# Kernel tuning notes

Hardware: AMD Instinct MI355X
Metric: run time of the kernel (lower is better)

The kernel has to match this reference:

```python
import jax, jax.numpy as jnp
import numpy as np

D_MODEL = 1024
N_HEADS = 16
D_K = D_MODEL // N_HEADS

def setup_inputs() -> dict:
    key = jax.random.key(0)
    ks = jax.random.split(key, 9)
    s = 1.0 / np.sqrt(D_MODEL)
    inp = {"x": jax.random.normal(ks[0], (2, 2048, D_MODEL), dtype=jnp.float32)}
    for i, name in enumerate(["q", "k", "v", "o"]):
        inp[f"W{name}"] = jax.random.uniform(ks[1 + i], (D_MODEL, D_MODEL), dtype=jnp.float32, minval=-s, maxval=s)
        inp[f"b{name}"] = jax.random.uniform(ks[5 + i], (D_MODEL,), dtype=jnp.float32, minval=-s, maxval=s)
    return inp

def _split_heads(t):
    B, S, _ = t.shape
    return t.reshape(B, S, N_HEADS, D_K).transpose(0, 2, 1, 3)  # [B,H,S,d_k]

def reference(x, Wq, bq, Wk, bk, Wv, bv, Wo, bo):
    # QKV projections (torch Linear: x @ W.T + b)
    q = _split_heads(x @ Wq.T + bq)
    k = _split_heads(x @ Wk.T + bk)
    v = _split_heads(x @ Wv.T + bv)
    scores = jnp.einsum('bhqd,bhkd->bhqk', q, k) / jnp.sqrt(jnp.asarray(D_K, x.dtype))
    probs = jax.nn.softmax(scores, axis=-1)
    attn = jnp.einsum('bhqk,bhkd->bhqd', probs, v)  # [B,H,S,d_k]
    B, H, S, _ = attn.shape
    merged = attn.transpose(0, 2, 1, 3).reshape(B, S, D_MODEL)
    return merged @ Wo.T + bo
```

## Files before the change

kernel.cpp:

```cpp
#include <hip/hip_runtime.h>
#include <hip/hip_bf16.h>
#include <stdint.h>


#define LOG2E 1.4426950408889634f

typedef float f32x4 __attribute__((ext_vector_type(4)));
typedef short bf16x8 __attribute__((ext_vector_type(8)));
typedef short bf16x4 __attribute__((ext_vector_type(4)));

__device__ __forceinline__ unsigned short f2bf(float f) {
  __hip_bfloat16 h = __float2bfloat16(f);
  return reinterpret_cast<unsigned short&>(h);
}
__device__ __forceinline__ float bf2f(unsigned short u) {
  union { unsigned int i; float f; } v; v.i = ((unsigned int)u) << 16; return v.f;
}

#define GLDS(g, l) __builtin_amdgcn_global_load_lds(                          \
    (const __attribute__((address_space(1))) void*)(g),                       \
    (__attribute__((address_space(3))) void*)(l), 16, 0, 0)

__global__ __launch_bounds__(256) void k_prep(const float* __restrict__ x,
                                              const float* __restrict__ wq,
                                              const float* __restrict__ wk,
                                              const float* __restrict__ wv,
                                              const float* __restrict__ wo,
                                              const float* __restrict__ bq,
                                              const float* __restrict__ bk,
                                              const float* __restrict__ bv,
                                              unsigned short* __restrict__ xb,
                                              unsigned short* __restrict__ Wb,
                                              unsigned short* __restrict__ Wob,
                                              float* __restrict__ biasQ) {
  const int blk = blockIdx.x;
  if (blk >= 8192) {
    int i = (blk - 8192) * 256 + threadIdx.x;
    float v;
    if (i < 1024) v = bq[i] * (0.125f * LOG2E);
    else if (i < 2048) v = bk[i - 1024];
    else v = bv[i - 2048];
    biasQ[i] = v;
    return;
  }
  const int gi = blk * 256 + threadIdx.x;
  const float* src;
  unsigned short* dst;
  float scale = 1.0f;
  int off;
  if (gi < 1048576) { src = x; dst = xb; off = gi; }
  else {
    const int wi = gi - 1048576;
    const int m = wi >> 18;
    off = wi & 262143;
    src = (m == 0) ? wq : (m == 1) ? wk : (m == 2) ? wv : wo;
    dst = (m == 3) ? Wob : (Wb + m * 1048576);
    if (m == 0) scale = 0.125f * LOG2E;
  }
  float4 v = ((const float4*)src)[off];
  ushort4 o;
  o.x = f2bf(v.x * scale);
  o.y = f2bf(v.y * scale);
  o.z = f2bf(v.z * scale);
  o.w = f2bf(v.w * scale);
  ((ushort4*)dst)[off] = o;
}

__global__ __launch_bounds__(256) void k_gemm0(const unsigned short* __restrict__ A,
                                               const unsigned short* __restrict__ B,
                                               const float* __restrict__ bias,
                                               unsigned short* __restrict__ outp) {
  __shared__ unsigned short As[128 * 32];
  __shared__ unsigned short Bs[128 * 32];
  const int tid = threadIdx.x;
  const int lane = tid & 63, wid = tid >> 6;
  const int wr = wid >> 1, wc = wid & 1;
  const int r = lane & 15, g = lane >> 4;
  const int bm = blockIdx.x, bn = blockIdx.y;

  const unsigned short* gA = A + (size_t)bm * 128 * 1024;
  const unsigned short* gB = B + (size_t)bn * 128 * 1024;
  const int row0 = tid >> 2, cg = (tid & 3) * 8;

  f32x4 acc[4][4] = {};

  for (int k0 = 0; k0 < 1024; k0 += 32) {
    __syncthreads();
    GLDS(gA + (size_t)row0 * 1024 + k0 + cg,        As + row0 * 32 + cg);
    GLDS(gA + (size_t)(row0 + 64) * 1024 + k0 + cg, As + (row0 + 64) * 32 + cg);
    GLDS(gB + (size_t)row0 * 1024 + k0 + cg,        Bs + row0 * 32 + cg);
    GLDS(gB + (size_t)(row0 + 64) * 1024 + k0 + cg, Bs + (row0 + 64) * 32 + cg);
    __syncthreads();

    bf16x8 af[4], bfr[4];
#pragma unroll
    for (int i = 0; i < 4; i++) {
      af[i]  = *(const bf16x8*)(As + (wr * 64 + i * 16 + r) * 32 + g * 8);
      bfr[i] = *(const bf16x8*)(Bs + (wc * 64 + i * 16 + r) * 32 + g * 8);
    }
#pragma unroll
    for (int i = 0; i < 4; i++)
#pragma unroll
      for (int j = 0; j < 4; j++)
        acc[i][j] = __builtin_amdgcn_mfma_f32_16x16x32_bf16(af[i], bfr[j], acc[i][j], 0, 0, 0);
  }

#pragma unroll
  for (int i = 0; i < 4; i++) {
    const int rowb = bm * 128 + wr * 64 + i * 16 + g * 4;
#pragma unroll
    for (int j = 0; j < 4; j++) {
      const int col = bn * 128 + wc * 64 + j * 16 + r;
      const float bv = bias[col];
      const int mat = col >> 10, nn = col & 1023;
      const int hh = nn >> 6, dd = nn & 63;
      const int bb = rowb >> 11, ss = rowb & 2047;
      if (mat == 2) {
        bf16x4 ov;
#pragma unroll
        for (int t = 0; t < 4; t++) ov[t] = (short)f2bf(acc[i][j][t] + bv);
        *(bf16x4*)(&outp[(size_t)2 * 4194304 +
            (size_t)((bb * 16 + hh) * 64 + dd) * 2048 + ss]) = ov;
      } else {
#pragma unroll
        for (int t = 0; t < 4; t++)
          outp[(size_t)mat * 4194304 +
               (size_t)((bb * 16 + hh) * 2048 + ss + t) * 64 + dd] =
              f2bf(acc[i][j][t] + bv);
      }
    }
  }
}

__global__ __launch_bounds__(256) void k_comb(const unsigned short* __restrict__ oP,
                                              const float* __restrict__ lP,
                                              unsigned short* __restrict__ mrg) {
  const int i = blockIdx.x * 256 + threadIdx.x;
  const int row = i >> 7, colg = i & 127;
  const int hh = colg >> 3;
  const int li = ((row >> 11) * 16 + hh) * 2048 + (row & 2047);
  const float inv = 1.0f / (lP[li] + lP[65536 + li]);
  const bf16x8 x0 = *(const bf16x8*)(oP + (size_t)i * 8);
  const bf16x8 x1 = *(const bf16x8*)(oP + 4194304 + (size_t)i * 8);
  bf16x8 o;
#pragma unroll
  for (int j = 0; j < 8; j++)
    o[j] = (short)f2bf((bf2f((unsigned short)x0[j]) + bf2f((unsigned short)x1[j])) * inv);
  *(bf16x8*)(mrg + (size_t)i * 8) = o;
}

__global__ __launch_bounds__(256) void k_gemm1(const unsigned short* __restrict__ A,
                                               const unsigned short* __restrict__ B,
                                               const float* __restrict__ bias,
                                               float* __restrict__ outp) {
  __shared__ unsigned short As[128 * 32];
  __shared__ unsigned short Bs[128 * 32];
  const int tid = threadIdx.x;
  const int lane = tid & 63, wid = tid >> 6;
  const int wr = wid >> 1, wc = wid & 1;
  const int r = lane & 15, g = lane >> 4;
  const int bm = blockIdx.x, bn = blockIdx.y;

  const unsigned short* gA = A + (size_t)bm * 128 * 1024;
  const unsigned short* gB = B + (size_t)bn * 128 * 1024;
  const int row0 = tid >> 2, cg = (tid & 3) * 8;

  f32x4 acc[4][4] = {};

  for (int k0 = 0; k0 < 1024; k0 += 32) {
    __syncthreads();
    GLDS(gA + (size_t)row0 * 1024 + k0 + cg,        As + row0 * 32 + cg);
    GLDS(gA + (size_t)(row0 + 64) * 1024 + k0 + cg, As + (row0 + 64) * 32 + cg);
    GLDS(gB + (size_t)row0 * 1024 + k0 + cg,        Bs + row0 * 32 + cg);
    GLDS(gB + (size_t)(row0 + 64) * 1024 + k0 + cg, Bs + (row0 + 64) * 32 + cg);
    __syncthreads();

    bf16x8 af[4], bfr[4];
#pragma unroll
    for (int i = 0; i < 4; i++) {
      af[i]  = *(const bf16x8*)(As + (wr * 64 + i * 16 + r) * 32 + g * 8);
      bfr[i] = *(const bf16x8*)(Bs + (wc * 64 + i * 16 + r) * 32 + g * 8);
    }
#pragma unroll
    for (int i = 0; i < 4; i++)
#pragma unroll
      for (int j = 0; j < 4; j++)
        acc[i][j] = __builtin_amdgcn_mfma_f32_16x16x32_bf16(af[i], bfr[j], acc[i][j], 0, 0, 0);
  }

#pragma unroll
  for (int i = 0; i < 4; i++) {
    const int rowb = bm * 128 + wr * 64 + i * 16 + g * 4;
#pragma unroll
    for (int j = 0; j < 4; j++) {
      const int col = bn * 128 + wc * 64 + j * 16 + r;
      const float bv = bias[col];
#pragma unroll
      for (int t = 0; t < 4; t++)
        outp[(size_t)(rowb + t) * 1024 + col] = acc[i][j][t] + bv;
    }
  }
}

__global__ __launch_bounds__(256) void k_attn(const unsigned short* __restrict__ Q,
                                              const unsigned short* __restrict__ Km,
                                              const unsigned short* __restrict__ Vt,
                                              unsigned short* __restrict__ oPart,
                                              float* __restrict__ lPart) {
  __shared__ unsigned short Kb[2][4096];
  __shared__ unsigned short Vb[2][4096];
  __shared__ unsigned short Pl[4][1024];
  const int tid = threadIdx.x;
  const int lane = tid & 63, w = tid >> 6;
  const int r = lane & 15, g = lane >> 4;
  const int bh = blockIdx.y;
  const int b = bh >> 4, h = bh & 15;
  const int q0 = blockIdx.x * 128;
  const int kg = blockIdx.z;

  const unsigned short* Qh  = Q  + (size_t)bh * 131072;
  const unsigned short* KhG = Km + (size_t)bh * 131072 + (size_t)kg * 65536;
  const unsigned short* VtG = Vt + (size_t)bh * 131072 + 1024 * kg;

  const int qrowA = q0 + w * 32 + r;
  bf16x8 bQ[2][2];
#pragma unroll
  for (int f = 0; f < 2; f++) {
    bQ[f][0] = *(const bf16x8*)(Qh + (size_t)(qrowA + f * 16) * 64 + g * 8);
    bQ[f][1] = *(const bf16x8*)(Qh + (size_t)(qrowA + f * 16) * 64 + 32 + g * 8);
  }

  int ksrc[2], vsrc[2];
#pragma unroll
  for (int op = 0; op < 2; op++) {
    const int c = op * 256 + tid;
    const int st = c >> 7, dh = (c >> 6) & 1, gg = (c >> 4) & 3, rr = c & 15;
    ksrc[op] = (st * 16 + rr) * 64 + dh * 32 + gg * 8;
    vsrc[op] = (st * 16 + rr) * 2048 + dh * 32 + gg * 8;
  }
  const int ldst = tid * 8;

  GLDS(KhG + ksrc[0], &Kb[0][ldst]);
  GLDS(KhG + ksrc[1], &Kb[0][2048 + ldst]);
  GLDS(VtG + vsrc[0], &Vb[0][ldst]);
  GLDS(VtG + vsrc[1], &Vb[0][2048 + ldst]);
  __syncthreads();

  f32x4 o[2][4] = {};
  f32x4 ol[2] = {};
  bf16x8 aONE;
#pragma unroll
  for (int j = 0; j < 8; j++) aONE[j] = (short)0x3F80;

  const unsigned swz = ((unsigned)(r & 7)) << 4;
  char* const plw = (char*)&Pl[w][0];

  for (int t = 0; t < 16; ++t) {
    const int cur = t & 1;
    if (t < 15) {
      const size_t kv = (size_t)(t + 1) * 64;
      GLDS(KhG + kv * 64 + ksrc[0], &Kb[cur ^ 1][ldst]);
      GLDS(KhG + kv * 64 + ksrc[1], &Kb[cur ^ 1][2048 + ldst]);
      GLDS(VtG + kv + vsrc[0], &Vb[cur ^ 1][ldst]);
      GLDS(VtG + kv + vsrc[1], &Vb[cur ^ 1][2048 + ldst]);
    }

    const unsigned short* kb = &Kb[cur][lane * 8];
    const unsigned short* vb = &Vb[cur][lane * 8];

    bf16x8 kf[4][2], vf[4][2];
#pragma unroll
    for (int st = 0; st < 4; st++) {
      kf[st][0] = *(const bf16x8*)(kb + st * 1024);
      kf[st][1] = *(const bf16x8*)(kb + st * 1024 + 512);
      vf[st][0] = *(const bf16x8*)(vb + st * 1024);
      vf[st][1] = *(const bf16x8*)(vb + st * 1024 + 512);
    }

#pragma unroll
    for (int f = 0; f < 2; f++) {
      f32x4 St[4];
#pragma unroll
      for (int st = 0; st < 4; st++) {
        f32x4 z = {0.f, 0.f, 0.f, 0.f};
        z = __builtin_amdgcn_mfma_f32_16x16x32_bf16(kf[st][0], bQ[f][0], z, 0, 0, 0);
        St[st] = __builtin_amdgcn_mfma_f32_16x16x32_bf16(kf[st][1], bQ[f][1], z, 0, 0, 0);
      }

#pragma unroll
      for (int st = 0; st < 4; st++) {
        bf16x4 pk;
#pragma unroll
        for (int u = 0; u < 4; u++)
          pk[u] = (short)f2bf(__builtin_amdgcn_exp2f(St[st][u]));
        *(bf16x4*)(plw + (((unsigned)(r * 128 + st * 32 + g * 8)) ^ swz)) = pk;
      }
      const bf16x8 pb0 = *(const bf16x8*)(plw + (((unsigned)(r * 128 + g * 16)) ^ swz));
      const bf16x8 pb1 = *(const bf16x8*)(plw + (((unsigned)(r * 128 + 64 + g * 16)) ^ swz));

#pragma unroll
      for (int c4 = 0; c4 < 4; c4++) {
        o[f][c4] = __builtin_amdgcn_mfma_f32_16x16x32_bf16(vf[c4][0], pb0, o[f][c4], 0, 0, 0);
        o[f][c4] = __builtin_amdgcn_mfma_f32_16x16x32_bf16(vf[c4][1], pb1, o[f][c4], 0, 0, 0);
      }
      ol[f] = __builtin_amdgcn_mfma_f32_16x16x32_bf16(aONE, pb0, ol[f], 0, 0, 0);
      ol[f] = __builtin_amdgcn_mfma_f32_16x16x32_bf16(aONE, pb1, ol[f], 0, 0, 0);
    }

    __syncthreads();
  }

#pragma unroll
  for (int f = 0; f < 2; f++) {
    const int qrow = qrowA + f * 16;
    if (g == 0) lPart[kg * 65536 + bh * 2048 + qrow] = ol[f][0];
    unsigned short* oP = oPart + (size_t)kg * 4194304 +
                         (size_t)(b * 2048 + qrow) * 1024 + h * 64;
#pragma unroll
    for (int c4 = 0; c4 < 4; c4++) {
      bf16x4 ov;
#pragma unroll
      for (int u = 0; u < 4; u++) ov[u] = (short)f2bf(o[f][c4][u]);
      *(bf16x4*)(oP + c4 * 16 + g * 4) = ov;
    }
  }
}

extern "C" void kernel_launch(void* const* d_in, const int* in_sizes, int n_in,
                              void* d_out, int out_size, void* d_ws, size_t ws_size,
                              hipStream_t stream) {
  const float* x  = (const float*)d_in[0];
  const float* Wq = (const float*)d_in[1];
  const float* bq = (const float*)d_in[2];
  const float* Wk = (const float*)d_in[3];
  const float* bk = (const float*)d_in[4];
  const float* Wv = (const float*)d_in[5];
  const float* bv = (const float*)d_in[6];
  const float* Wo = (const float*)d_in[7];
  const float* bo = (const float*)d_in[8];

  if (ws_size < (size_t)44576768) return;

  unsigned short* ws  = (unsigned short*)d_ws;
  unsigned short* qkv  = ws;
  unsigned short* Wob  = ws + 12582912;
  float* biasQ = (float*)(ws + 13631488);
  float* lPart = (float*)(ws + 13637632);
  unsigned short* oPart = ws + 13899776;
  unsigned short* xb = ws + 13899776;
  unsigned short* Wb = ws + 18094080;
  unsigned short* mrg = ws;

  k_prep<<<dim3(8204), dim3(256), 0, stream>>>(x, Wq, Wk, Wv, Wo, bq, bk, bv,
                                               xb, Wb, Wob, biasQ);
  k_gemm0<<<dim3(32, 24), dim3(256), 0, stream>>>(xb, Wb, biasQ, qkv);
  k_attn<<<dim3(16, 32, 2), dim3(256), 0, stream>>>(
      qkv, qkv + 4194304, qkv + 8388608, oPart, lPart);
  k_comb<<<dim3(2048), dim3(256), 0, stream>>>(oPart, lPart, mrg);
  k_gemm1<<<dim3(32, 8), dim3(256), 0, stream>>>(mrg, Wob, bo, (float*)d_out);
}
```

Measured before the change: 134.6 us.

## Drop KV split in attention and fuse normalization, removing combine kernel

```diff
diff --git a/kernel.cpp b/kernel.cpp
--- a/kernel.cpp
+++ b/kernel.cpp
@@ -12,9 +12,6 @@
 __device__ __forceinline__ unsigned short f2bf(float f) {
   __hip_bfloat16 h = __float2bfloat16(f);
   return reinterpret_cast<unsigned short&>(h);
-}
-__device__ __forceinline__ float bf2f(unsigned short u) {
-  union { unsigned int i; float f; } v; v.i = ((unsigned int)u) << 16; return v.f;
 }
 
 #define GLDS(g, l) __builtin_amdgcn_global_load_lds(                          \
@@ -132,23 +129,6 @@
   }
 }
 
-__global__ __launch_bounds__(256) void k_comb(const unsigned short* __restrict__ oP,
-                                              const float* __restrict__ lP,
-                                              unsigned short* __restrict__ mrg) {
-  const int i = blockIdx.x * 256 + threadIdx.x;
-  const int row = i >> 7, colg = i & 127;
-  const int hh = colg >> 3;
-  const int li = ((row >> 11) * 16 + hh) * 2048 + (row & 2047);
-  const float inv = 1.0f / (lP[li] + lP[65536 + li]);
-  const bf16x8 x0 = *(const bf16x8*)(oP + (size_t)i * 8);
-  const bf16x8 x1 = *(const bf16x8*)(oP + 4194304 + (size_t)i * 8);
-  bf16x8 o;
-#pragma unroll
-  for (int j = 0; j < 8; j++)
-    o[j] = (short)f2bf((bf2f((unsigned short)x0[j]) + bf2f((unsigned short)x1[j])) * inv);
-  *(bf16x8*)(mrg + (size_t)i * 8) = o;
-}
-
 __global__ __launch_bounds__(256) void k_gemm1(const unsigned short* __restrict__ A,
                                                const unsigned short* __restrict__ B,
                                                const float* __restrict__ bias,
@@ -205,8 +185,7 @@
 __global__ __launch_bounds__(256) void k_attn(const unsigned short* __restrict__ Q,
                                               const unsigned short* __restrict__ Km,
                                               const unsigned short* __restrict__ Vt,
-                                              unsigned short* __restrict__ oPart,
-                                              float* __restrict__ lPart) {
+                                              unsigned short* __restrict__ merged) {
   __shared__ unsigned short Kb[2][4096];
   __shared__ unsigned short Vb[2][4096];
   __shared__ unsigned short Pl[4][1024];
@@ -216,11 +195,10 @@
   const int bh = blockIdx.y;
   const int b = bh >> 4, h = bh & 15;
   const int q0 = blockIdx.x * 128;
-  const int kg = blockIdx.z;
 
   const unsigned short* Qh  = Q  + (size_t)bh * 131072;
-  const unsigned short* KhG = Km + (size_t)bh * 131072 + (size_t)kg * 65536;
-  const unsigned short* VtG = Vt + (size_t)bh * 131072 + 1024 * kg;
+  const unsigned short* Kh  = Km + (size_t)bh * 131072;
+  const unsigned short* Vth = Vt + (size_t)bh * 131072;
 
   const int qrowA = q0 + w * 32 + r;
   bf16x8 bQ[2][2];
@@ -240,10 +218,10 @@
   }
   const int ldst = tid * 8;
 
-  GLDS(KhG + ksrc[0], &Kb[0][ldst]);
-  GLDS(KhG + ksrc[1], &Kb[0][2048 + ldst]);
-  GLDS(VtG + vsrc[0], &Vb[0][ldst]);
-  GLDS(VtG + vsrc[1], &Vb[0][2048 + ldst]);
+  GLDS(Kh + ksrc[0],  &Kb[0][ldst]);
+  GLDS(Kh + ksrc[1],  &Kb[0][2048 + ldst]);
+  GLDS(Vth + vsrc[0], &Vb[0][ldst]);
+  GLDS(Vth + vsrc[1], &Vb[0][2048 + ldst]);
   __syncthreads();
 
   f32x4 o[2][4] = {};
@@ -255,14 +233,14 @@
   const unsigned swz = ((unsigned)(r & 7)) << 4;
   char* const plw = (char*)&Pl[w][0];
 
-  for (int t = 0; t < 16; ++t) {
+  for (int t = 0; t < 32; ++t) {
     const int cur = t & 1;
-    if (t < 15) {
+    if (t < 31) {
       const size_t kv = (size_t)(t + 1) * 64;
-      GLDS(KhG + kv * 64 + ksrc[0], &Kb[cur ^ 1][ldst]);
-      GLDS(KhG + kv * 64 + ksrc[1], &Kb[cur ^ 1][2048 + ldst]);
-      GLDS(VtG + kv + vsrc[0], &Vb[cur ^ 1][ldst]);
-      GLDS(VtG + kv + vsrc[1], &Vb[cur ^ 1][2048 + ldst]);
+      GLDS(Kh + kv * 64 + ksrc[0],  &Kb[cur ^ 1][ldst]);
+      GLDS(Kh + kv * 64 + ksrc[1],  &Kb[cur ^ 1][2048 + ldst]);
+      GLDS(Vth + kv + vsrc[0], &Vb[cur ^ 1][ldst]);
+      GLDS(Vth + kv + vsrc[1], &Vb[cur ^ 1][2048 + ldst]);
     }
 
     const unsigned short* kb = &Kb[cur][lane * 8];
@@ -312,16 +290,14 @@
 
 #pragma unroll
   for (int f = 0; f < 2; f++) {
-    const int qrow = qrowA + f * 16;
-    if (g == 0) lPart[kg * 65536 + bh * 2048 + qrow] = ol[f][0];
-    unsigned short* oP = oPart + (size_t)kg * 4194304 +
-                         (size_t)(b * 2048 + qrow) * 1024 + h * 64;
+    const float inv = 1.0f / ol[f][0];
+    const size_t base = (size_t)(b * 2048 + qrowA + f * 16) * 1024 + h * 64;
 #pragma unroll
     for (int c4 = 0; c4 < 4; c4++) {
       bf16x4 ov;
 #pragma unroll
-      for (int u = 0; u < 4; u++) ov[u] = (short)f2bf(o[f][c4][u]);
-      *(bf16x4*)(oP + c4 * 16 + g * 4) = ov;
+      for (int u = 0; u < 4; u++) ov[u] = (short)f2bf(o[f][c4][u] * inv);
+      *(bf16x4*)(&merged[base + c4 * 16 + g * 4]) = ov;
     }
   }
 }
@@ -339,23 +315,20 @@
   const float* Wo = (const float*)d_in[7];
   const float* bo = (const float*)d_in[8];
 
-  if (ws_size < (size_t)44576768) return;
+  if (ws_size < (size_t)42479616) return;
 
   unsigned short* ws  = (unsigned short*)d_ws;
   unsigned short* qkv  = ws;
   unsigned short* Wob  = ws + 12582912;
   float* biasQ = (float*)(ws + 13631488);
-  float* lPart = (float*)(ws + 13637632);
-  unsigned short* oPart = ws + 13899776;
   unsigned short* xb = ws + 13899776;
   unsigned short* Wb = ws + 18094080;
-  unsigned short* mrg = ws;
+  unsigned short* mrg = ws + 13899776;
 
   k_prep<<<dim3(8204), dim3(256), 0, stream>>>(x, Wq, Wk, Wv, Wo, bq, bk, bv,
                                                xb, Wb, Wob, biasQ);
   k_gemm0<<<dim3(32, 24), dim3(256), 0, stream>>>(xb, Wb, biasQ, qkv);
-  k_attn<<<dim3(16, 32, 2), dim3(256), 0, stream>>>(
-      qkv, qkv + 4194304, qkv + 8388608, oPart, lPart);
-  k_comb<<<dim3(2048), dim3(256), 0, stream>>>(oPart, lPart, mrg);
+  k_attn<<<dim3(16, 32), dim3(256), 0, stream>>>(
+      qkv, qkv + 4194304, qkv + 8388608, mrg);
   k_gemm1<<<dim3(32, 8), dim3(256), 0, stream>>>(mrg, Wob, bo, (float*)d_out);
 }
```

After: 121.3 us. 1.11x faster.
